# Kernel tuning notes

Hardware: AMD Instinct MI355X
Metric: run time of the kernel (lower is better)

Reference implementation:

```python
import jax, jax.numpy as jnp
import numpy as np

B, C, H, N, M = 4, 256, 4, 2048, 2048
D = C // H  # head_dim
BN_EPS = 1e-5


def conv1x1(W, b, x):
    # nn.Conv1d(Cin, Cout, kernel_size=1): x [B, Cin, N] -> [B, Cout, N]
    return jnp.einsum('oc,bcn->bon', W, x) + b[None, :, None]


def setup_inputs() -> dict:
    key = jax.random.key(0)
    ks = jax.random.split(key, 10)
    w = lambda k, shape: (jax.random.normal(k, shape, jnp.float32) * 0.05)
    return {
        'x1': jax.random.normal(ks[0], (B, C, N), jnp.float32),
        'x2': jax.random.normal(ks[1], (B, C, M), jnp.float32),
        'kv_mask': jax.random.randint(ks[2], (B, M), 0, 2).astype(bool),
        'Wq': w(ks[3], (C, C)), 'bq': jnp.zeros((C,), jnp.float32),
        'Wk': w(ks[4], (C, C)), 'bk': jnp.zeros((C,), jnp.float32),
        'Wv': w(ks[5], (C, C)), 'bv': jnp.zeros((C,), jnp.float32),
        'Wmh': w(ks[6], (C, C)), 'bmh': jnp.zeros((C,), jnp.float32),
        'W1': w(ks[7], (2 * C, 2 * C)), 'b1': jnp.zeros((2 * C,), jnp.float32),
        'bn_gamma': jnp.ones((2 * C,), jnp.float32),
        'bn_beta': jnp.zeros((2 * C,), jnp.float32),
        'bn_mean': jnp.zeros((2 * C,), jnp.float32),
        'bn_var': jnp.ones((2 * C,), jnp.float32),
        'W2': w(ks[8], (C, 2 * C)), 'b2': jnp.zeros((C,), jnp.float32),
    }


def reference(x1, x2, kv_mask, Wq, bq, Wk, bk, Wv, bv, Wmh, bmh,
              W1, b1, bn_gamma, bn_beta, bn_mean, bn_var, W2, b2):
    bsz = x1.shape[0]
    # 1x1-conv Q/K/V projections, reshaped to [B, H, D, N]
    q = conv1x1(Wq, bq, x1).reshape(bsz, H, D, -1)
    k = conv1x1(Wk, bk, x2).reshape(bsz, H, D, -1)
    v = conv1x1(Wv, bv, x2).reshape(bsz, H, D, -1)

    # full attention: scores [B, H, N, M]
    QK = jnp.einsum('bhdn,bhdm->bhnm', q, k)
    # masked_fill happens BEFORE the 1/sqrt(D) scaling in the original
    QK = jnp.where(kv_mask[:, None, None, :], QK, jnp.float32(-1e6))
    score = jax.nn.softmax(QK / np.float32(np.sqrt(D)), axis=-1)
    add_value = jnp.einsum('bhnm,bhdm->bhdn', score, v).reshape(bsz, H * D, -1)

    add_value = conv1x1(Wmh, bmh, add_value)

    # cat_filter: conv1x1 -> BatchNorm1d (inference stats) -> ReLU -> conv1x1
    cat = jnp.concatenate([x1, add_value], axis=1)  # [B, 2C, N]
    h = conv1x1(W1, b1, cat)
    h = (h - bn_mean[None, :, None]) / jnp.sqrt(bn_var[None, :, None] + BN_EPS)
    h = bn_gamma[None, :, None] * h + bn_beta[None, :, None]
    h = jax.nn.relu(h)
    return x1 + conv1x1(W2, b2, h)
```

## Files before the change

### kernel.cpp

```cpp
#include <hip/hip_runtime.h>
#include <hip/hip_bf16.h>

#define SEQN 2048
#define SEQM 2048
#define CDIM 256
#define NB   4
#define NH   4

using bf16x8 = __attribute__((ext_vector_type(8))) short;
using f32x4  = __attribute__((ext_vector_type(4))) float;

__device__ inline unsigned short f2bf(float x) {
    __hip_bfloat16 h = __float2bfloat16(x);
    return *reinterpret_cast<unsigned short*>(&h);
}

__global__ __launch_bounds__(256) void prep_k(
    const int* __restrict__ kvm, int* __restrict__ pidx, int* __restrict__ mcnt,
    const float* __restrict__ W1, const float* __restrict__ b1,
    const float* __restrict__ gamma, const float* __restrict__ beta,
    const float* __restrict__ mean, const float* __restrict__ var,
    const float* __restrict__ Wmh, const float* __restrict__ bmh,
    unsigned short* __restrict__ Acat, float* __restrict__ cvec,
    const float* __restrict__ Wq, const float* __restrict__ Wk,
    const float* __restrict__ Wv, const float* __restrict__ W2,
    unsigned short* __restrict__ Wqb, unsigned short* __restrict__ Wkb,
    unsigned short* __restrict__ Wvb, unsigned short* __restrict__ W2b,
    const float* __restrict__ x1, const float* __restrict__ x2,
    unsigned short* __restrict__ catT, unsigned short* __restrict__ x2T)
{
    __shared__ float smemf[64 * 68];
    const int bid = blockIdx.x, tid = threadIdx.x;

    if (bid < NB) {
        int* sc = reinterpret_cast<int*>(smemf);
        const int b = bid;
        int loc[8], c = 0;
        #pragma unroll
        for (int e = 0; e < 8; ++e) {
            loc[e] = (kvm[(size_t)b * SEQM + tid * 8 + e] != 0) ? 1 : 0;
            c += loc[e];
        }
        sc[tid] = c;
        __syncthreads();
        for (int off = 1; off < 256; off <<= 1) {
            int v = (tid >= off) ? sc[tid - off] : 0;
            __syncthreads();
            sc[tid] += v;
            __syncthreads();
        }
        int p = sc[tid] - c;
        if (tid == 255) mcnt[b] = sc[255];
        #pragma unroll
        for (int e = 0; e < 8; ++e) {
            pidx[(size_t)b * SEQM + tid * 8 + e] = loc[e] ? p : -1;
            p += loc[e];
        }
    } else if (bid < NB + 512) {
        const int j = bid - NB;
        const int c = tid;
        const float s = gamma[j] * rsqrtf(var[j] + 1e-5f);
        const float* w1b = W1 + (size_t)j * 512 + 256;
        Acat[(size_t)j * 512 + c] = f2bf(s * W1[(size_t)j * 512 + c]);
        float acc = 0.f;
        for (int t = 0; t < 256; ++t)
            acc += w1b[t] * Wmh[(size_t)t * 256 + c];
        Acat[(size_t)j * 512 + 256 + c] = f2bf(s * acc);
        if (c == 0) {
            float ab = 0.f;
            for (int t = 0; t < 256; ++t) ab += w1b[t] * bmh[t];
            cvec[j] = s * (b1[j] + ab - mean[j]) + beta[j];
        }
    } else if (bid < NB + 512 + 320) {
        int cid = bid - (NB + 512);
        const float* src; unsigned short* dst; int n;
        if (cid < 64)       { src = Wq; dst = Wqb; n = 65536; }
        else if (cid < 128) { src = Wk; dst = Wkb; n = 65536;  cid -= 64;  }
        else if (cid < 192) { src = Wv; dst = Wvb; n = 65536;  cid -= 128; }
        else                { src = W2; dst = W2b; n = 131072; cid -= 192; }
        const int idx = (cid * 256 + tid) * 4;
        if (idx < n) {
            float4 v = *reinterpret_cast<const float4*>(&src[idx]);
            ushort4 p; p.x = f2bf(v.x); p.y = f2bf(v.y); p.z = f2bf(v.z); p.w = f2bf(v.w);
            *reinterpret_cast<ushort4*>(&dst[idx]) = p;
        }
    } else {
        int t = bid - (NB + 512 + 320);
        const float* src; unsigned short* dst; int ldd;
        if (t < 512) { src = x1; dst = catT; ldd = 512; }
        else         { src = x2; dst = x2T;  ldd = 256; t -= 512; }
        const int cx = t & 3, ny = (t >> 2) & 31, b = t >> 7;
        const int c0 = cx * 64, n0 = ny * 64;
        float (*Ts)[68] = reinterpret_cast<float(*)[68]>(smemf);
        const int cr = tid >> 2, nc = (tid & 3) * 16;
        #pragma unroll
        for (int q = 0; q < 4; ++q) {
            float4 v = *reinterpret_cast<const float4*>(
                &src[((size_t)b * CDIM + c0 + cr) * SEQN + n0 + nc + 4 * q]);
            *reinterpret_cast<float4*>(&Ts[cr][nc + 4 * q]) = v;
        }
        __syncthreads();
        const int nr = tid >> 2, cc = (tid & 3) * 16;
        unsigned short tmp[16];
        #pragma unroll
        for (int e = 0; e < 16; ++e) tmp[e] = f2bf(Ts[cc + e][nr]);
        unsigned short* dp = &dst[((size_t)(b * SEQN + n0 + nr)) * ldd + c0 + cc];
        #pragma unroll
        for (int q = 0; q < 4; ++q)
            *reinterpret_cast<ushort4*>(&dp[4 * q]) = *reinterpret_cast<ushort4*>(&tmp[4 * q]);
    }
}

__global__ __launch_bounds__(256) void qkv_gemm_k(
    const unsigned short* __restrict__ Wqb, const unsigned short* __restrict__ Wkb,
    const unsigned short* __restrict__ Wvb,
    const unsigned short* __restrict__ catT, const unsigned short* __restrict__ x2T,
    const float* __restrict__ bq, const float* __restrict__ bk,
    const float* __restrict__ bv,
    unsigned short* __restrict__ qbf, unsigned short* __restrict__ kbf,
    unsigned short* __restrict__ vbf,
    const int* __restrict__ pidx, float qscale)
{
    __shared__ short At[128][72];
    __shared__ short Bt[64][72];
    const int z = blockIdx.z;
    const unsigned short* W = (z == 0) ? Wqb : (z == 1) ? Wkb : Wvb;
    const unsigned short* X = (z == 0) ? catT : x2T;
    const float* bias = (z == 0) ? bq : (z == 1) ? bk : bv;
    const int ldx = (z == 0) ? 512 : 256;

    const int tid = threadIdx.x;
    const int w = tid >> 6, l = tid & 63, lm = l & 15, lg = l >> 4;
    const int o0 = blockIdx.x * 128, ng0 = blockIdx.y * 64;
    const int wo = (w >> 1) * 64, wn = (w & 1) * 32;

    f32x4 acc[4][2] = {};
    const int arow = tid >> 2, acol = (tid & 3) * 16;

    for (int k0 = 0; k0 < 256; k0 += 64) {
        __syncthreads();
        #pragma unroll
        for (int p = 0; p < 2; ++p) {
            const unsigned short* s = &W[(size_t)(o0 + arow + 64 * p) * 256 + k0 + acol];
            *reinterpret_cast<bf16x8*>(&At[arow + 64 * p][acol]) =
                *reinterpret_cast<const bf16x8*>(s);
            *reinterpret_cast<bf16x8*>(&At[arow + 64 * p][acol + 8]) =
                *reinterpret_cast<const bf16x8*>(s + 8);
        }
        {
            const unsigned short* s = &X[(size_t)(ng0 + arow) * ldx + k0 + acol];
            *reinterpret_cast<bf16x8*>(&Bt[arow][acol]) =
                *reinterpret_cast<const bf16x8*>(s);
            *reinterpret_cast<bf16x8*>(&Bt[arow][acol + 8]) =
                *reinterpret_cast<const bf16x8*>(s + 8);
        }
        __syncthreads();
        #pragma unroll
        for (int kc = 0; kc < 2; ++kc) {
            bf16x8 a[4], bf[2];
            #pragma unroll
            for (int i = 0; i < 4; ++i)
                a[i] = *reinterpret_cast<const bf16x8*>(&At[wo + 16 * i + lm][kc * 32 + lg * 8]);
            #pragma unroll
            for (int j = 0; j < 2; ++j)
                bf[j] = *reinterpret_cast<const bf16x8*>(&Bt[wn + 16 * j + lm][kc * 32 + lg * 8]);
            #pragma unroll
            for (int i = 0; i < 4; ++i)
                #pragma unroll
                for (int j = 0; j < 2; ++j)
                    acc[i][j] = __builtin_amdgcn_mfma_f32_16x16x32_bf16(a[i], bf[j], acc[i][j], 0, 0, 0);
        }
    }

    #pragma unroll
    for (int j = 0; j < 2; ++j) {
        const int ng = ng0 + wn + 16 * j + lm;
        const int b = ng >> 11, n = ng & 2047;
        const int pos = (z == 0) ? n : pidx[(size_t)b * SEQM + n];
        #pragma unroll
        for (int i = 0; i < 4; ++i) {
            const int ob = o0 + wo + 16 * i + 4 * lg;
            float4 bv4 = *reinterpret_cast<const float4*>(&bias[ob]);
            float v[4] = {acc[i][j][0] + bv4.x, acc[i][j][1] + bv4.y,
                          acc[i][j][2] + bv4.z, acc[i][j][3] + bv4.w};
            if (z == 2) {
                if (pos >= 0) {
                    #pragma unroll
                    for (int r = 0; r < 4; ++r)
                        vbf[((size_t)b * CDIM + ob + r) * SEQM + pos] = f2bf(v[r]);
                }
            } else if (pos >= 0) {
                const int hh = ob >> 6, dbase = ob & 63;
                const float sc_ = (z == 0) ? qscale : 1.0f;
                ushort4 pk;
                pk.x = f2bf(v[0] * sc_); pk.y = f2bf(v[1] * sc_);
                pk.z = f2bf(v[2] * sc_); pk.w = f2bf(v[3] * sc_);
                unsigned short* dst = (z == 0) ? qbf : kbf;
                *reinterpret_cast<ushort4*>(
                    &dst[(((size_t)b * NH + hh) * SEQN + pos) * 64 + dbase]) = pk;
            }
        }
    }
}

template<int OMODE>
__global__ __launch_bounds__(256) void gemm_mfma_k(
    const unsigned short* __restrict__ W, const unsigned short* __restrict__ X,
    const float* __restrict__ bias, const float* __restrict__ res,
    unsigned short* __restrict__ obf, float* __restrict__ ofp,
    const int* __restrict__ pidx, int K, int ldx, float oscale)
{
    __shared__ short At[128][72];
    __shared__ short Bt[64][72];
    const int tid = threadIdx.x;
    const int w = tid >> 6, l = tid & 63, lm = l & 15, lg = l >> 4;
    const int o0 = blockIdx.x * 128, ng0 = blockIdx.y * 64;
    const int wo = (w >> 1) * 64, wn = (w & 1) * 32;

    f32x4 acc[4][2] = {};
    const int arow = tid >> 2, acol = (tid & 3) * 16;

    for (int k0 = 0; k0 < K; k0 += 64) {
        __syncthreads();
        #pragma unroll
        for (int p = 0; p < 2; ++p) {
            const unsigned short* s = &W[(size_t)(o0 + arow + 64 * p) * K + k0 + acol];
            *reinterpret_cast<bf16x8*>(&At[arow + 64 * p][acol]) =
                *reinterpret_cast<const bf16x8*>(s);
            *reinterpret_cast<bf16x8*>(&At[arow + 64 * p][acol + 8]) =
                *reinterpret_cast<const bf16x8*>(s + 8);
        }
        {
            const unsigned short* s = &X[(size_t)(ng0 + arow) * ldx + k0 + acol];
            *reinterpret_cast<bf16x8*>(&Bt[arow][acol]) =
                *reinterpret_cast<const bf16x8*>(s);
            *reinterpret_cast<bf16x8*>(&Bt[arow][acol + 8]) =
                *reinterpret_cast<const bf16x8*>(s + 8);
        }
        __syncthreads();
        #pragma unroll
        for (int kc = 0; kc < 2; ++kc) {
            bf16x8 a[4], bf[2];
            #pragma unroll
            for (int i = 0; i < 4; ++i)
                a[i] = *reinterpret_cast<const bf16x8*>(&At[wo + 16 * i + lm][kc * 32 + lg * 8]);
            #pragma unroll
            for (int j = 0; j < 2; ++j)
                bf[j] = *reinterpret_cast<const bf16x8*>(&Bt[wn + 16 * j + lm][kc * 32 + lg * 8]);
            #pragma unroll
            for (int i = 0; i < 4; ++i)
                #pragma unroll
                for (int j = 0; j < 2; ++j)
                    acc[i][j] = __builtin_amdgcn_mfma_f32_16x16x32_bf16(a[i], bf[j], acc[i][j], 0, 0, 0);
        }
    }

    #pragma unroll
    for (int j = 0; j < 2; ++j) {
        const int ng = ng0 + wn + 16 * j + lm;
        const int b = ng >> 11, n = ng & 2047;
        #pragma unroll
        for (int i = 0; i < 4; ++i) {
            const int ob = o0 + wo + 16 * i + 4 * lg;
            float4 bv = *reinterpret_cast<const float4*>(&bias[ob]);
            float v[4] = {acc[i][j][0] + bv.x, acc[i][j][1] + bv.y,
                          acc[i][j][2] + bv.z, acc[i][j][3] + bv.w};
            if (OMODE == 2) {
                ushort4 pk;
                pk.x = f2bf(fmaxf(v[0], 0.f)); pk.y = f2bf(fmaxf(v[1], 0.f));
                pk.z = f2bf(fmaxf(v[2], 0.f)); pk.w = f2bf(fmaxf(v[3], 0.f));
                *reinterpret_cast<ushort4*>(&obf[(size_t)ng * 512 + ob]) = pk;
            } else {
                #pragma unroll
                for (int r = 0; r < 4; ++r) {
                    size_t ad = ((size_t)b * CDIM + ob + r) * SEQN + n;
                    ofp[ad] = v[r] + res[ad];
                }
            }
        }
    }
}

__global__ __launch_bounds__(256) void attn_mfma_k(
    const unsigned short* __restrict__ qbf, const unsigned short* __restrict__ kbf,
    const unsigned short* __restrict__ vbf, const int* __restrict__ mcntg,
    unsigned short* __restrict__ catT)
{
    __shared__ short Ks[2][64][64];
    __shared__ short Vs[2][64][64];
    __shared__ unsigned int Ps[4][16][36];

    const int tid = threadIdx.x;
    const int w = tid >> 6, l = tid & 63;
    const int lm = l & 15, lg = l >> 4;
    const int h = blockIdx.y, b = blockIdx.z;
    const int n_base = blockIdx.x * 64 + w * 16;
    const size_t bhN = (size_t)(b * NH + h) * SEQN;
    const size_t cBase = (size_t)b * CDIM + h * 64;

    const int mcnt = mcntg[b];
    const int ntiles = (mcnt + 63) >> 6;

    if (ntiles == 0) {
        #pragma unroll
        for (int r = 0; r < 4; ++r) {
            int n = n_base + 4 * lg + r;
            unsigned short* dst = &catT[((size_t)b * SEQN + n) * 512 + 256 + h * 64];
            #pragma unroll
            for (int t = 0; t < 4; ++t) dst[16 * t + lm] = 0;
        }
        return;
    }

    const size_t qrow = (bhN + n_base + lm) * 64;
    bf16x8 qa0 = *reinterpret_cast<const bf16x8*>(&qbf[qrow + lg * 8]);
    bf16x8 qa1 = *reinterpret_cast<const bf16x8*>(&qbf[qrow + 32 + lg * 8]);

    f32x4 oacc[4] = {};
    float mrun = -3.0e5f, lrun = 0.f;

    const int r0 = tid >> 3, c8 = (tid & 7) * 8;
    const int c8s = c8 ^ ((r0 & 7) << 3);
    const int colr0 = (lg * 8) ^ ((lm & 7) << 3);
    const int colr1 = (32 + lg * 8) ^ ((lm & 7) << 3);

    {
        bf16x8 kr[2], vr[2];
        #pragma unroll
        for (int p = 0; p < 2; ++p) {
            kr[p] = *reinterpret_cast<const bf16x8*>(&kbf[(bhN + r0 + 32 * p) * 64 + c8]);
            vr[p] = *reinterpret_cast<const bf16x8*>(&vbf[(cBase + r0 + 32 * p) * SEQM + c8]);
        }
        #pragma unroll
        for (int p = 0; p < 2; ++p) {
            *reinterpret_cast<bf16x8*>(&Ks[0][r0 + 32 * p][c8s]) = kr[p];
            *reinterpret_cast<bf16x8*>(&Vs[0][r0 + 32 * p][c8s]) = vr[p];
        }
    }
    __syncthreads();

    for (int t64 = 0; t64 < ntiles; ++t64) {
        const int cur = t64 & 1;
        const bool has_next = (t64 < ntiles - 1);
        const int m0n = (t64 + 1) * 64;

        bf16x8 kr[2], vr[2];
        if (has_next) {
            #pragma unroll
            for (int p = 0; p < 2; ++p) {
                kr[p] = *reinterpret_cast<const bf16x8*>(
                    &kbf[(bhN + m0n + r0 + 32 * p) * 64 + c8]);
                vr[p] = *reinterpret_cast<const bf16x8*>(
                    &vbf[(cBase + r0 + 32 * p) * SEQM + m0n + c8]);
            }
        }

        f32x4 sv[4];
        __builtin_amdgcn_s_setprio(1);
        #pragma unroll
        for (int t = 0; t < 4; ++t) {
            bf16x8 ka0 = *reinterpret_cast<const bf16x8*>(&Ks[cur][16 * t + lm][colr0]);
            bf16x8 ka1 = *reinterpret_cast<const bf16x8*>(&Ks[cur][16 * t + lm][colr1]);
            f32x4 z = {0.f, 0.f, 0.f, 0.f};
            z = __builtin_amdgcn_mfma_f32_16x16x32_bf16(ka0, qa0, z, 0, 0, 0);
            z = __builtin_amdgcn_mfma_f32_16x16x32_bf16(ka1, qa1, z, 0, 0, 0);
            sv[t] = z;
        }
        __builtin_amdgcn_s_setprio(0);

        float mx = fmaxf(fmaxf(fmaxf(sv[0][0], sv[0][1]), fmaxf(sv[0][2], sv[0][3])),
                         fmaxf(fmaxf(sv[1][0], sv[1][1]), fmaxf(sv[1][2], sv[1][3])));
        mx = fmaxf(mx, fmaxf(fmaxf(fmaxf(sv[2][0], sv[2][1]), fmaxf(sv[2][2], sv[2][3])),
                             fmaxf(fmaxf(sv[3][0], sv[3][1]), fmaxf(sv[3][2], sv[3][3]))));
        mx = fmaxf(mx, __shfl_xor(mx, 16));
        mx = fmaxf(mx, __shfl_xor(mx, 32));
        const bool grew = (mx > mrun);
        float mnew = fmaxf(mrun, mx);
        float scl = exp2f(mrun - mnew);
        mrun = mnew;

        float rsum = 0.f;
        const int mrem = mcnt - t64 * 64;
        if (mrem >= 64) {
            #pragma unroll
            for (int t = 0; t < 4; ++t) {
                float p0 = exp2f(sv[t][0] - mnew);
                float p1 = exp2f(sv[t][1] - mnew);
                float p2 = exp2f(sv[t][2] - mnew);
                float p3 = exp2f(sv[t][3] - mnew);
                rsum += (p0 + p1) + (p2 + p3);
                unsigned int u0 = __builtin_amdgcn_perm(
                    __float_as_uint(p1), __float_as_uint(p0), 0x07060302u);
                unsigned int u1 = __builtin_amdgcn_perm(
                    __float_as_uint(p3), __float_as_uint(p2), 0x07060302u);
                *reinterpret_cast<uint2*>(&Ps[w][lm][8 * t + 2 * lg]) = make_uint2(u0, u1);
            }
        } else {
            #pragma unroll
            for (int t = 0; t < 4; ++t) {
                const int mb = 16 * t + 4 * lg;
                float p0 = (mb + 0 < mrem) ? exp2f(sv[t][0] - mnew) : 0.f;
                float p1 = (mb + 1 < mrem) ? exp2f(sv[t][1] - mnew) : 0.f;
                float p2 = (mb + 2 < mrem) ? exp2f(sv[t][2] - mnew) : 0.f;
                float p3 = (mb + 3 < mrem) ? exp2f(sv[t][3] - mnew) : 0.f;
                rsum += (p0 + p1) + (p2 + p3);
                unsigned int u0 = __builtin_amdgcn_perm(
                    __float_as_uint(p1), __float_as_uint(p0), 0x07060302u);
                unsigned int u1 = __builtin_amdgcn_perm(
                    __float_as_uint(p3), __float_as_uint(p2), 0x07060302u);
                *reinterpret_cast<uint2*>(&Ps[w][lm][8 * t + 2 * lg]) = make_uint2(u0, u1);
            }
        }
        rsum += __shfl_xor(rsum, 16);
        rsum += __shfl_xor(rsum, 32);
        lrun = lrun * scl + rsum;

        if (__any(grew && scl < 1.f)) {
            float sr[4];
            #pragma unroll
            for (int r = 0; r < 4; ++r) sr[r] = __shfl(scl, 4 * lg + r);
            #pragma unroll
            for (int t = 0; t < 4; ++t)
                #pragma unroll
                for (int r = 0; r < 4; ++r)
                    oacc[t][r] *= sr[r];
        }

        bf16x8 pa0 = *reinterpret_cast<const bf16x8*>(&Ps[w][lm][4 * lg]);
        bf16x8 pa1 = *reinterpret_cast<const bf16x8*>(&Ps[w][lm][16 + 4 * lg]);
        __builtin_amdgcn_s_setprio(1);
        #pragma unroll
        for (int t = 0; t < 4; ++t) {
            bf16x8 vb0 = *reinterpret_cast<const bf16x8*>(&Vs[cur][16 * t + lm][colr0]);
            bf16x8 vb1 = *reinterpret_cast<const bf16x8*>(&Vs[cur][16 * t + lm][colr1]);
            oacc[t] = __builtin_amdgcn_mfma_f32_16x16x32_bf16(pa0, vb0, oacc[t], 0, 0, 0);
            oacc[t] = __builtin_amdgcn_mfma_f32_16x16x32_bf16(pa1, vb1, oacc[t], 0, 0, 0);
        }
        __builtin_amdgcn_s_setprio(0);

        if (has_next) {
            const int nxt = cur ^ 1;
            #pragma unroll
            for (int p = 0; p < 2; ++p) {
                *reinterpret_cast<bf16x8*>(&Ks[nxt][r0 + 32 * p][c8s]) = kr[p];
                *reinterpret_cast<bf16x8*>(&Vs[nxt][r0 + 32 * p][c8s]) = vr[p];
            }
        }
        __syncthreads();
    }

    #pragma unroll
    for (int r = 0; r < 4; ++r) {
        float rinv = 1.f / __shfl(lrun, 4 * lg + r);
        int n = n_base + 4 * lg + r;
        unsigned short* dst = &catT[((size_t)b * SEQN + n) * 512 + 256 + h * 64];
        #pragma unroll
        for (int t = 0; t < 4; ++t)
            dst[16 * t + lm] = f2bf(oacc[t][r] * rinv);
    }
}

extern "C" void kernel_launch(void* const* d_in, const int* in_sizes, int n_in,
                              void* d_out, int out_size, void* d_ws, size_t ws_size,
                              hipStream_t stream)
{
    (void)in_sizes; (void)n_in; (void)out_size; (void)ws_size;
    const float* x1    = (const float*)d_in[0];
    const float* x2    = (const float*)d_in[1];
    const int*   kvm   = (const int*)  d_in[2];
    const float* Wq    = (const float*)d_in[3];
    const float* bq    = (const float*)d_in[4];
    const float* Wk    = (const float*)d_in[5];
    const float* bk    = (const float*)d_in[6];
    const float* Wv    = (const float*)d_in[7];
    const float* bv    = (const float*)d_in[8];
    const float* Wmh   = (const float*)d_in[9];
    const float* bmh   = (const float*)d_in[10];
    const float* W1    = (const float*)d_in[11];
    const float* b1    = (const float*)d_in[12];
    const float* gamma = (const float*)d_in[13];
    const float* beta  = (const float*)d_in[14];
    const float* mean  = (const float*)d_in[15];
    const float* var   = (const float*)d_in[16];
    const float* W2    = (const float*)d_in[17];
    const float* b2    = (const float*)d_in[18];
    float* out = (float*)d_out;

    const size_t act = (size_t)NB * CDIM * SEQN;
    unsigned short* ws   = (unsigned short*)d_ws;
    unsigned short* qbf  = ws;
    unsigned short* kbf  = qbf  + act;
    unsigned short* vbf  = kbf  + act;
    unsigned short* x2T  = vbf  + act;
    unsigned short* catT = x2T  + act;
    unsigned short* hbuf = catT + 2 * act;
    unsigned short* Wqb  = hbuf + 2 * act;
    unsigned short* Wkb  = Wqb  + 65536;
    unsigned short* Wvb  = Wkb  + 65536;
    unsigned short* W2b  = Wvb  + 65536;
    unsigned short* Acat = W2b  + 131072;
    float*          cvec = (float*)(Acat + 262144);
    int*            pidx = (int*)(cvec + 512);
    int*            mcnt = pidx + (size_t)NB * SEQM;

    const float qscale = 0.125f * 1.44269504088896f;

    prep_k<<<dim3(NB + 512 + 320 + 1024), dim3(256), 0, stream>>>(
        kvm, pidx, mcnt,
        W1, b1, gamma, beta, mean, var, Wmh, bmh, Acat, cvec,
        Wq, Wk, Wv, W2, Wqb, Wkb, Wvb, W2b,
        x1, x2, catT, x2T);

    qkv_gemm_k<<<dim3(2, 128, 3), dim3(256), 0, stream>>>(
        Wqb, Wkb, Wvb, catT, x2T, bq, bk, bv, qbf, kbf, vbf, pidx, qscale);

    attn_mfma_k<<<dim3(SEQN / 64, NH, NB), dim3(256), 0, stream>>>(
        qbf, kbf, vbf, mcnt, catT);

    gemm_mfma_k<2><<<dim3(4, 128), dim3(256), 0, stream>>>(
        Acat, catT, cvec, nullptr, hbuf, nullptr, nullptr, 512, 512, 1.0f);

    gemm_mfma_k<3><<<dim3(2, 128), dim3(256), 0, stream>>>(
        W2b, hbuf, b2, x1, nullptr, out, nullptr, 512, 512, 1.0f);
}
```

Baseline: 83.31 us.

## Fuse input transpose into QKV GEMM and merge the two cat-filter GEMMs

The QKV projection kernel now reads fp32 x1/x2 directly into a swizzled shared tile and converts to bf16 while building MFMA operands. This removes the separate transpose pass in prep_k and its catT/x2T round-trip through memory. Attention output now goes to a compact attnT buffer. A new single kernel per 32-column block stages x1 and attnT, runs the W1 GEMM with BN+ReLU into hbuf, then runs the W2 GEMM with bias and residual, replacing two launches. The trade-off is that the fused kernel has fewer, longer blocks that reload weight tiles without pipelining, and it reads hbuf back from global memory inside the block.

Result: slower. 109.9 us (+32.0%).

```diff
diff --git a/kernel.cpp b/kernel.cpp
--- a/kernel.cpp
+++ b/kernel.cpp
@@ -25,15 +25,12 @@
     const float* __restrict__ Wq, const float* __restrict__ Wk,
     const float* __restrict__ Wv, const float* __restrict__ W2,
     unsigned short* __restrict__ Wqb, unsigned short* __restrict__ Wkb,
-    unsigned short* __restrict__ Wvb, unsigned short* __restrict__ W2b,
-    const float* __restrict__ x1, const float* __restrict__ x2,
-    unsigned short* __restrict__ catT, unsigned short* __restrict__ x2T)
+    unsigned short* __restrict__ Wvb, unsigned short* __restrict__ W2b)
 {
-    __shared__ float smemf[64 * 68];
+    __shared__ int sc[256];
     const int bid = blockIdx.x, tid = threadIdx.x;
 
     if (bid < NB) {
-        int* sc = reinterpret_cast<int*>(smemf);
         const int b = bid;
         int loc[8], c = 0;
         #pragma unroll
@@ -71,50 +68,24 @@
             for (int t = 0; t < 256; ++t) ab += w1b[t] * bmh[t];
             cvec[j] = s * (b1[j] + ab - mean[j]) + beta[j];
         }
-    } else if (bid < NB + 512 + 320) {
+    } else {
         int cid = bid - (NB + 512);
-        const float* src; unsigned short* dst; int n;
-        if (cid < 64)       { src = Wq; dst = Wqb; n = 65536; }
-        else if (cid < 128) { src = Wk; dst = Wkb; n = 65536;  cid -= 64;  }
-        else if (cid < 192) { src = Wv; dst = Wvb; n = 65536;  cid -= 128; }
-        else                { src = W2; dst = W2b; n = 131072; cid -= 192; }
+        const float* src; unsigned short* dst;
+        if (cid < 64)       { src = Wq; dst = Wqb; }
+        else if (cid < 128) { src = Wk; dst = Wkb; cid -= 64;  }
+        else if (cid < 192) { src = Wv; dst = Wvb; cid -= 128; }
+        else                { src = W2; dst = W2b; cid -= 192; }
         const int idx = (cid * 256 + tid) * 4;
-        if (idx < n) {
-            float4 v = *reinterpret_cast<const float4*>(&src[idx]);
-            ushort4 p; p.x = f2bf(v.x); p.y = f2bf(v.y); p.z = f2bf(v.z); p.w = f2bf(v.w);
-            *reinterpret_cast<ushort4*>(&dst[idx]) = p;
-        }
-    } else {
-        int t = bid - (NB + 512 + 320);
-        const float* src; unsigned short* dst; int ldd;
-        if (t < 512) { src = x1; dst = catT; ldd = 512; }
-        else         { src = x2; dst = x2T;  ldd = 256; t -= 512; }
-        const int cx = t & 3, ny = (t >> 2) & 31, b = t >> 7;
-        const int c0 = cx * 64, n0 = ny * 64;
-        float (*Ts)[68] = reinterpret_cast<float(*)[68]>(smemf);
-        const int cr = tid >> 2, nc = (tid & 3) * 16;
-        #pragma unroll
-        for (int q = 0; q < 4; ++q) {
-            float4 v = *reinterpret_cast<const float4*>(
-                &src[((size_t)b * CDIM + c0 + cr) * SEQN + n0 + nc + 4 * q]);
-            *reinterpret_cast<float4*>(&Ts[cr][nc + 4 * q]) = v;
-        }
-        __syncthreads();
-        const int nr = tid >> 2, cc = (tid & 3) * 16;
-        unsigned short tmp[16];
-        #pragma unroll
-        for (int e = 0; e < 16; ++e) tmp[e] = f2bf(Ts[cc + e][nr]);
-        unsigned short* dp = &dst[((size_t)(b * SEQN + n0 + nr)) * ldd + c0 + cc];
-        #pragma unroll
-        for (int q = 0; q < 4; ++q)
-            *reinterpret_cast<ushort4*>(&dp[4 * q]) = *reinterpret_cast<ushort4*>(&tmp[4 * q]);
+        float4 v = *reinterpret_cast<const float4*>(&src[idx]);
+        ushort4 p; p.x = f2bf(v.x); p.y = f2bf(v.y); p.z = f2bf(v.z); p.w = f2bf(v.w);
+        *reinterpret_cast<ushort4*>(&dst[idx]) = p;
     }
 }
 
-__global__ __launch_bounds__(256) void qkv_gemm_k(
+__global__ __launch_bounds__(256) void qkv_k(
     const unsigned short* __restrict__ Wqb, const unsigned short* __restrict__ Wkb,
     const unsigned short* __restrict__ Wvb,
-    const unsigned short* __restrict__ catT, const unsigned short* __restrict__ x2T,
+    const float* __restrict__ x1, const float* __restrict__ x2,
     const float* __restrict__ bq, const float* __restrict__ bk,
     const float* __restrict__ bv,
     unsigned short* __restrict__ qbf, unsigned short* __restrict__ kbf,
@@ -122,20 +93,22 @@
     const int* __restrict__ pidx, float qscale)
 {
     __shared__ short At[128][72];
-    __shared__ short Bt[64][72];
+    __shared__ float Ts[64][68];
     const int z = blockIdx.z;
     const unsigned short* W = (z == 0) ? Wqb : (z == 1) ? Wkb : Wvb;
-    const unsigned short* X = (z == 0) ? catT : x2T;
+    const float* X = (z == 0) ? x1 : x2;
     const float* bias = (z == 0) ? bq : (z == 1) ? bk : bv;
-    const int ldx = (z == 0) ? 512 : 256;
 
     const int tid = threadIdx.x;
     const int w = tid >> 6, l = tid & 63, lm = l & 15, lg = l >> 4;
     const int o0 = blockIdx.x * 128, ng0 = blockIdx.y * 64;
+    const int b = ng0 >> 11, n0 = ng0 & 2047;
     const int wo = (w >> 1) * 64, wn = (w & 1) * 32;
 
     f32x4 acc[4][2] = {};
     const int arow = tid >> 2, acol = (tid & 3) * 16;
+    const int tr = tid >> 2, tc = (tid & 3) * 16;
+    const int tg = (((tc >> 4) ^ ((tr >> 3) & 3)) << 4);
 
     for (int k0 = 0; k0 < 256; k0 += 64) {
         __syncthreads();
@@ -148,11 +121,11 @@
                 *reinterpret_cast<const bf16x8*>(s + 8);
         }
         {
-            const unsigned short* s = &X[(size_t)(ng0 + arow) * ldx + k0 + acol];
-            *reinterpret_cast<bf16x8*>(&Bt[arow][acol]) =
-                *reinterpret_cast<const bf16x8*>(s);
-            *reinterpret_cast<bf16x8*>(&Bt[arow][acol + 8]) =
-                *reinterpret_cast<const bf16x8*>(s + 8);
+            const float* s = &X[((size_t)b * CDIM + k0 + tr) * SEQN + n0 + tc];
+            #pragma unroll
+            for (int q = 0; q < 4; ++q)
+                *reinterpret_cast<float4*>(&Ts[tr][tg + 4 * q]) =
+                    *reinterpret_cast<const float4*>(&s[4 * q]);
         }
         __syncthreads();
         #pragma unroll
@@ -162,8 +135,18 @@
             for (int i = 0; i < 4; ++i)
                 a[i] = *reinterpret_cast<const bf16x8*>(&At[wo + 16 * i + lm][kc * 32 + lg * 8]);
             #pragma unroll
-            for (int j = 0; j < 2; ++j)
-                bf[j] = *reinterpret_cast<const bf16x8*>(&Bt[wn + 16 * j + lm][kc * 32 + lg * 8]);
+            for (int j = 0; j < 2; ++j) {
+                const int bk0 = kc * 32 + lg * 8;
+                const int gcol = (((((wn >> 4) + j)) ^ ((bk0 >> 3) & 3)) << 4) | lm;
+                union { unsigned int u[4]; bf16x8 v; } cv;
+                #pragma unroll
+                for (int e = 0; e < 4; ++e) {
+                    float lo = Ts[bk0 + 2 * e][gcol];
+                    float hi = Ts[bk0 + 2 * e + 1][gcol];
+                    cv.u[e] = (unsigned int)f2bf(lo) | ((unsigned int)f2bf(hi) << 16);
+                }
+                bf[j] = cv.v;
+            }
             #pragma unroll
             for (int i = 0; i < 4; ++i)
                 #pragma unroll
@@ -175,8 +158,8 @@
     #pragma unroll
     for (int j = 0; j < 2; ++j) {
         const int ng = ng0 + wn + 16 * j + lm;
-        const int b = ng >> 11, n = ng & 2047;
-        const int pos = (z == 0) ? n : pidx[(size_t)b * SEQM + n];
+        const int bb = ng >> 11, n = ng & 2047;
+        const int pos = (z == 0) ? n : pidx[(size_t)bb * SEQM + n];
         #pragma unroll
         for (int i = 0; i < 4; ++i) {
             const int ob = o0 + wo + 16 * i + 4 * lg;
@@ -187,7 +170,7 @@
                 if (pos >= 0) {
                     #pragma unroll
                     for (int r = 0; r < 4; ++r)
-                        vbf[((size_t)b * CDIM + ob + r) * SEQM + pos] = f2bf(v[r]);
+                        vbf[((size_t)bb * CDIM + ob + r) * SEQM + pos] = f2bf(v[r]);
                 }
             } else if (pos >= 0) {
                 const int hh = ob >> 6, dbase = ob & 63;
@@ -197,85 +180,7 @@
                 pk.z = f2bf(v[2] * sc_); pk.w = f2bf(v[3] * sc_);
                 unsigned short* dst = (z == 0) ? qbf : kbf;
                 *reinterpret_cast<ushort4*>(
-                    &dst[(((size_t)b * NH + hh) * SEQN + pos) * 64 + dbase]) = pk;
-            }
-        }
-    }
-}
-
-template<int OMODE>
-__global__ __launch_bounds__(256) void gemm_mfma_k(
-    const unsigned short* __restrict__ W, const unsigned short* __restrict__ X,
-    const float* __restrict__ bias, const float* __restrict__ res,
-    unsigned short* __restrict__ obf, float* __restrict__ ofp,
-    const int* __restrict__ pidx, int K, int ldx, float oscale)
-{
-    __shared__ short At[128][72];
-    __shared__ short Bt[64][72];
-    const int tid = threadIdx.x;
-    const int w = tid >> 6, l = tid & 63, lm = l & 15, lg = l >> 4;
-    const int o0 = blockIdx.x * 128, ng0 = blockIdx.y * 64;
-    const int wo = (w >> 1) * 64, wn = (w & 1) * 32;
-
-    f32x4 acc[4][2] = {};
-    const int arow = tid >> 2, acol = (tid & 3) * 16;
-
-    for (int k0 = 0; k0 < K; k0 += 64) {
-        __syncthreads();
-        #pragma unroll
-        for (int p = 0; p < 2; ++p) {
-            const unsigned short* s = &W[(size_t)(o0 + arow + 64 * p) * K + k0 + acol];
-            *reinterpret_cast<bf16x8*>(&At[arow + 64 * p][acol]) =
-                *reinterpret_cast<const bf16x8*>(s);
-            *reinterpret_cast<bf16x8*>(&At[arow + 64 * p][acol + 8]) =
-                *reinterpret_cast<const bf16x8*>(s + 8);
-        }
-        {
-            const unsigned short* s = &X[(size_t)(ng0 + arow) * ldx + k0 + acol];
-            *reinterpret_cast<bf16x8*>(&Bt[arow][acol]) =
-                *reinterpret_cast<const bf16x8*>(s);
-            *reinterpret_cast<bf16x8*>(&Bt[arow][acol + 8]) =
-                *reinterpret_cast<const bf16x8*>(s + 8);
-        }
-        __syncthreads();
-        #pragma unroll
-        for (int kc = 0; kc < 2; ++kc) {
-            bf16x8 a[4], bf[2];
-            #pragma unroll
-            for (int i = 0; i < 4; ++i)
-                a[i] = *reinterpret_cast<const bf16x8*>(&At[wo + 16 * i + lm][kc * 32 + lg * 8]);
-            #pragma unroll
-            for (int j = 0; j < 2; ++j)
-                bf[j] = *reinterpret_cast<const bf16x8*>(&Bt[wn + 16 * j + lm][kc * 32 + lg * 8]);
-            #pragma unroll
-            for (int i = 0; i < 4; ++i)
-                #pragma unroll
-                for (int j = 0; j < 2; ++j)
-                    acc[i][j] = __builtin_amdgcn_mfma_f32_16x16x32_bf16(a[i], bf[j], acc[i][j], 0, 0, 0);
-        }
-    }
-
-    #pragma unroll
-    for (int j = 0; j < 2; ++j) {
-        const int ng = ng0 + wn + 16 * j + lm;
-        const int b = ng >> 11, n = ng & 2047;
-        #pragma unroll
-        for (int i = 0; i < 4; ++i) {
-            const int ob = o0 + wo + 16 * i + 4 * lg;
-            float4 bv = *reinterpret_cast<const float4*>(&bias[ob]);
-            float v[4] = {acc[i][j][0] + bv.x, acc[i][j][1] + bv.y,
-                          acc[i][j][2] + bv.z, acc[i][j][3] + bv.w};
-            if (OMODE == 2) {
-                ushort4 pk;
-                pk.x = f2bf(fmaxf(v[0], 0.f)); pk.y = f2bf(fmaxf(v[1], 0.f));
-                pk.z = f2bf(fmaxf(v[2], 0.f)); pk.w = f2bf(fmaxf(v[3], 0.f));
-                *reinterpret_cast<ushort4*>(&obf[(size_t)ng * 512 + ob]) = pk;
-            } else {
-                #pragma unroll
-                for (int r = 0; r < 4; ++r) {
-                    size_t ad = ((size_t)b * CDIM + ob + r) * SEQN + n;
-                    ofp[ad] = v[r] + res[ad];
-                }
+                    &dst[(((size_t)bb * NH + hh) * SEQN + pos) * 64 + dbase]) = pk;
             }
         }
     }
@@ -284,7 +189,7 @@
 __global__ __launch_bounds__(256) void attn_mfma_k(
     const unsigned short* __restrict__ qbf, const unsigned short* __restrict__ kbf,
     const unsigned short* __restrict__ vbf, const int* __restrict__ mcntg,
-    unsigned short* __restrict__ catT)
+    unsigned short* __restrict__ attnT)
 {
     __shared__ short Ks[2][64][64];
     __shared__ short Vs[2][64][64];
@@ -305,7 +210,7 @@
         #pragma unroll
         for (int r = 0; r < 4; ++r) {
             int n = n_base + 4 * lg + r;
-            unsigned short* dst = &catT[((size_t)b * SEQN + n) * 512 + 256 + h * 64];
+            unsigned short* dst = &attnT[((size_t)b * SEQN + n) * 256 + h * 64];
             #pragma unroll
             for (int t = 0; t < 4; ++t) dst[16 * t + lm] = 0;
         }
@@ -453,10 +358,123 @@
     for (int r = 0; r < 4; ++r) {
         float rinv = 1.f / __shfl(lrun, 4 * lg + r);
         int n = n_base + 4 * lg + r;
-        unsigned short* dst = &catT[((size_t)b * SEQN + n) * 512 + 256 + h * 64];
+        unsigned short* dst = &attnT[((size_t)b * SEQN + n) * 256 + h * 64];
         #pragma unroll
         for (int t = 0; t < 4; ++t)
             dst[16 * t + lm] = f2bf(oacc[t][r] * rinv);
+    }
+}
+
+__global__ __launch_bounds__(256) void gemm23_k(
+    const unsigned short* __restrict__ Acat, const float* __restrict__ cvec,
+    const unsigned short* __restrict__ W2b, const float* __restrict__ b2,
+    const float* __restrict__ x1, const unsigned short* __restrict__ attnT,
+    unsigned short* __restrict__ hbuf, float* __restrict__ out)
+{
+    __shared__ short At[128][72];
+    __shared__ short Bc[32][520];
+
+    const int tid = threadIdx.x;
+    const int w = tid >> 6, l = tid & 63, lm = l & 15, lg = l >> 4;
+    const int blk = blockIdx.x;
+    const int b = blk >> 6, n0 = (blk & 63) * 32;
+    const size_t bng = (size_t)b * SEQN + n0;
+
+    {
+        const int nr = tid & 31, kg = tid >> 3 >> 2;
+        #pragma unroll
+        for (int kk = 0; kk < 32; kk += 2) {
+            float f0 = x1[((size_t)b * CDIM + kg * 32 + kk) * SEQN + n0 + nr];
+            float f1 = x1[((size_t)b * CDIM + kg * 32 + kk + 1) * SEQN + n0 + nr];
+            *reinterpret_cast<unsigned int*>(&Bc[nr][kg * 32 + kk]) =
+                (unsigned int)f2bf(f0) | ((unsigned int)f2bf(f1) << 16);
+        }
+        const unsigned short* ar = &attnT[(bng + nr) * 256 + kg * 32];
+        #pragma unroll
+        for (int e = 0; e < 4; ++e)
+            *reinterpret_cast<bf16x8*>(&Bc[nr][256 + kg * 32 + 8 * e]) =
+                *reinterpret_cast<const bf16x8*>(&ar[8 * e]);
+    }
+
+    const int arow = tid >> 2, acol = (tid & 3) * 16;
+    const int wo = (w >> 1) * 64, wn = (w & 1) * 16;
+
+    for (int ob = 0; ob < 4; ++ob) {
+        const int o0 = ob * 128;
+        f32x4 acc[4] = {};
+        for (int k0 = 0; k0 < 512; k0 += 64) {
+            __syncthreads();
+            #pragma unroll
+            for (int p = 0; p < 2; ++p) {
+                const unsigned short* s = &Acat[(size_t)(o0 + arow + 64 * p) * 512 + k0 + acol];
+                *reinterpret_cast<bf16x8*>(&At[arow + 64 * p][acol]) =
+                    *reinterpret_cast<const bf16x8*>(s);
+                *reinterpret_cast<bf16x8*>(&At[arow + 64 * p][acol + 8]) =
+                    *reinterpret_cast<const bf16x8*>(s + 8);
+            }
+            __syncthreads();
+            #pragma unroll
+            for (int kc = 0; kc < 2; ++kc) {
+                bf16x8 a[4];
+                #pragma unroll
+                for (int i = 0; i < 4; ++i)
+                    a[i] = *reinterpret_cast<const bf16x8*>(&At[wo + 16 * i + lm][kc * 32 + lg * 8]);
+                bf16x8 bfr = *reinterpret_cast<const bf16x8*>(&Bc[wn + lm][k0 + kc * 32 + lg * 8]);
+                #pragma unroll
+                for (int i = 0; i < 4; ++i)
+                    acc[i] = __builtin_amdgcn_mfma_f32_16x16x32_bf16(a[i], bfr, acc[i], 0, 0, 0);
+            }
+        }
+        #pragma unroll
+        for (int i = 0; i < 4; ++i) {
+            const int o = o0 + wo + 16 * i + 4 * lg;
+            float4 cv = *reinterpret_cast<const float4*>(&cvec[o]);
+            ushort4 pk;
+            pk.x = f2bf(fmaxf(acc[i][0] + cv.x, 0.f));
+            pk.y = f2bf(fmaxf(acc[i][1] + cv.y, 0.f));
+            pk.z = f2bf(fmaxf(acc[i][2] + cv.z, 0.f));
+            pk.w = f2bf(fmaxf(acc[i][3] + cv.w, 0.f));
+            *reinterpret_cast<ushort4*>(&hbuf[(bng + wn + lm) * 512 + o]) = pk;
+        }
+    }
+
+    for (int ob = 0; ob < 2; ++ob) {
+        const int o0 = ob * 128;
+        f32x4 acc[4] = {};
+        for (int k0 = 0; k0 < 512; k0 += 64) {
+            __syncthreads();
+            #pragma unroll
+            for (int p = 0; p < 2; ++p) {
+                const unsigned short* s = &W2b[(size_t)(o0 + arow + 64 * p) * 512 + k0 + acol];
+                *reinterpret_cast<bf16x8*>(&At[arow + 64 * p][acol]) =
+                    *reinterpret_cast<const bf16x8*>(s);
+                *reinterpret_cast<bf16x8*>(&At[arow + 64 * p][acol + 8]) =
+                    *reinterpret_cast<const bf16x8*>(s + 8);
+            }
+            __syncthreads();
+            #pragma unroll
+            for (int kc = 0; kc < 2; ++kc) {
+                bf16x8 a[4];
+                #pragma unroll
+                for (int i = 0; i < 4; ++i)
+                    a[i] = *reinterpret_cast<const bf16x8*>(&At[wo + 16 * i + lm][kc * 32 + lg * 8]);
+                bf16x8 bfr = *reinterpret_cast<const bf16x8*>(
+                    &hbuf[(bng + wn + lm) * 512 + k0 + kc * 32 + lg * 8]);
+                #pragma unroll
+                for (int i = 0; i < 4; ++i)
+                    acc[i] = __builtin_amdgcn_mfma_f32_16x16x32_bf16(a[i], bfr, acc[i], 0, 0, 0);
+            }
+        }
+        #pragma unroll
+        for (int i = 0; i < 4; ++i) {
+            const int o = o0 + wo + 16 * i + 4 * lg;
+            float4 bv4 = *reinterpret_cast<const float4*>(&b2[o]);
+            #pragma unroll
+            for (int r = 0; r < 4; ++r) {
+                size_t ad = ((size_t)b * CDIM + o + r) * SEQN + n0 + wn + lm;
+                out[ad] = acc[i][r] + ((const float*)&bv4)[r] + x1[ad];
+            }
+        }
     }
 }
 
@@ -487,39 +505,33 @@
     float* out = (float*)d_out;
 
     const size_t act = (size_t)NB * CDIM * SEQN;
-    unsigned short* ws   = (unsigned short*)d_ws;
-    unsigned short* qbf  = ws;
-    unsigned short* kbf  = qbf  + act;
-    unsigned short* vbf  = kbf  + act;
-    unsigned short* x2T  = vbf  + act;
-    unsigned short* catT = x2T  + act;
-    unsigned short* hbuf = catT + 2 * act;
-    unsigned short* Wqb  = hbuf + 2 * act;
-    unsigned short* Wkb  = Wqb  + 65536;
-    unsigned short* Wvb  = Wkb  + 65536;
-    unsigned short* W2b  = Wvb  + 65536;
-    unsigned short* Acat = W2b  + 131072;
-    float*          cvec = (float*)(Acat + 262144);
-    int*            pidx = (int*)(cvec + 512);
-    int*            mcnt = pidx + (size_t)NB * SEQM;
+    unsigned short* ws    = (unsigned short*)d_ws;
+    unsigned short* qbf   = ws;
+    unsigned short* kbf   = qbf   + act;
+    unsigned short* vbf   = kbf   + act;
+    unsigned short* attnT = vbf   + act;
+    unsigned short* hbuf  = attnT + act;
+    unsigned short* Wqb   = hbuf  + 2 * act;
+    unsigned short* Wkb   = Wqb   + 65536;
+    unsigned short* Wvb   = Wkb   + 65536;
+    unsigned short* W2b   = Wvb   + 65536;
+    unsigned short* Acat  = W2b   + 131072;
+    float*          cvec  = (float*)(Acat + 262144);
+    int*            pidx  = (int*)(cvec + 512);
+    int*            mcnt  = pidx + (size_t)NB * SEQM;
 
     const float qscale = 0.125f * 1.44269504088896f;
 
-    prep_k<<<dim3(NB + 512 + 320 + 1024), dim3(256), 0, stream>>>(
-        kvm, pidx, mcnt,
-        W1, b1, gamma, beta, mean, var, Wmh, bmh, Acat, cvec,
-        Wq, Wk, Wv, W2, Wqb, Wkb, Wvb, W2b,
-        x1, x2, catT, x2T);
-
-    qkv_gemm_k<<<dim3(2, 128, 3), dim3(256), 0, stream>>>(
-        Wqb, Wkb, Wvb, catT, x2T, bq, bk, bv, qbf, kbf, vbf, pidx, qscale);
+    prep_k<<<dim3(836), dim3(256), 0, stream>>>(
+        kvm, pidx, mcnt, W1, b1, gamma, beta, mean, var, Wmh, bmh,
+        Acat, cvec, Wq, Wk, Wv, W2, Wqb, Wkb, Wvb, W2b);
+
+    qkv_k<<<dim3(2, 128, 3), dim3(256), 0, stream>>>(
+        Wqb, Wkb, Wvb, x1, x2, bq, bk, bv, qbf, kbf, vbf, pidx, qscale);
 
     attn_mfma_k<<<dim3(SEQN / 64, NH, NB), dim3(256), 0, stream>>>(
-        qbf, kbf, vbf, mcnt, catT);
-
-    gemm_mfma_k<2><<<dim3(4, 128), dim3(256), 0, stream>>>(
-        Acat, catT, cvec, nullptr, hbuf, nullptr, nullptr, 512, 512, 1.0f);
-
-    gemm_mfma_k<3><<<dim3(2, 128), dim3(256), 0, stream>>>(
-        W2b, hbuf, b2, x1, nullptr, out, nullptr, 512, 512, 1.0f);
+        qbf, kbf, vbf, mcnt, attnT);
+
+    gemm23_k<<<dim3(256), dim3(256), 0, stream>>>(
+        Acat, cvec, W2b, b2, x1, attnT, hbuf, out);
 }
```
